# Optimization experiments

Measured on AMD Instinct MI355X. Metric: run time of the kernel, lower is better.

Reference implementation:

```python
import jax, jax.numpy as jnp
import numpy as np

N_NODES = 50000
N_EDGES = 1600000
IN_CH = 256
LAT = 32
HID = 64
OUT_CH = 256
GAT_H = 32  # GAT hidden dims [32, 32], heads=1


def setup_inputs() -> dict:
    key = jax.random.key(0)
    ks = jax.random.split(key, 30)
    nrm = lambda k, shape, s=0.05: jax.random.normal(k, shape, dtype=jnp.float32) * s
    inp = {}
    inp["x"] = jax.random.normal(ks[0], (N_NODES, IN_CH), dtype=jnp.float32)
    inp["edge_index"] = jax.random.randint(ks[1], (2, N_EDGES), 0, N_NODES)
    # GAT layer 1: IN_CH -> 32 (heads=1), layer 2: 32 -> 32, final linear 32 -> LAT
    inp["W_g1"] = nrm(ks[2], (IN_CH, GAT_H)); inp["as_g1"] = nrm(ks[3], (GAT_H,)); inp["ad_g1"] = nrm(ks[4], (GAT_H,)); inp["b_g1"] = jnp.zeros((GAT_H,), jnp.float32)
    inp["W_g2"] = nrm(ks[5], (GAT_H, GAT_H)); inp["as_g2"] = nrm(ks[6], (GAT_H,)); inp["ad_g2"] = nrm(ks[7], (GAT_H,)); inp["b_g2"] = jnp.zeros((GAT_H,), jnp.float32)
    inp["W_gf"] = nrm(ks[8], (GAT_H, LAT)); inp["b_gf"] = jnp.zeros((LAT,), jnp.float32)
    inp["W_m1"] = nrm(ks[9], (IN_CH, HID)); inp["b_m1"] = jnp.zeros((HID,), jnp.float32); inp["g_m1"] = jnp.ones((HID,), jnp.float32); inp["be_m1"] = jnp.zeros((HID,), jnp.float32)
    inp["W_m2"] = nrm(ks[10], (HID, HID)); inp["b_m2"] = jnp.zeros((HID,), jnp.float32); inp["g_m2"] = jnp.ones((HID,), jnp.float32); inp["be_m2"] = jnp.zeros((HID,), jnp.float32)
    inp["W_m3"] = nrm(ks[11], (HID, LAT)); inp["b_m3"] = jnp.zeros((LAT,), jnp.float32); inp["g_m3"] = jnp.ones((LAT,), jnp.float32); inp["be_m3"] = jnp.zeros((LAT,), jnp.float32)
    # final linear LAT -> OUT_CH + ReLU
    inp["W_f"] = nrm(ks[12], (LAT, OUT_CH)); inp["b_f"] = jnp.zeros((OUT_CH,), jnp.float32)
    return inp


def _bn_relu(h, g, b):
    # BatchNorm1d in training mode: batch stats, biased variance, eps=1e-5
    m = jnp.mean(h, axis=0)
    v = jnp.var(h, axis=0)
    return jax.nn.relu((h - m) * jax.lax.rsqrt(v + 1e-5) * g + b)


def _gat(h_in, src, dst, W, a_s, a_d, b):
    # PyG GATConv (heads=1): edge (src j -> dst i), e = LeakyReLU(a_src.Wx_j + a_dst.Wx_i)
    N = h_in.shape[0]
    h = h_in @ W                                   # [N, F]
    e = jax.nn.leaky_relu((h @ a_s)[src] + (h @ a_d)[dst], 0.2)  # [E]
    m = jax.ops.segment_max(e, dst, num_segments=N)              # scatter-softmax over incoming edges
    ex = jnp.exp(e - m[dst])
    den = jax.ops.segment_sum(ex, dst, num_segments=N)
    alpha = ex / den[dst]
    out = jax.ops.segment_sum(alpha[:, None] * h[src], dst, num_segments=N)
    return out + b


def reference(x, edge_index, W_g1, as_g1, ad_g1, b_g1, W_g2, as_g2, ad_g2, b_g2, W_gf, b_gf, W_m1, b_m1, g_m1, be_m1, W_m2, b_m2, g_m2, be_m2, W_m3, b_m3, g_m3, be_m3, W_f, b_f):
    N = x.shape[0]
    loops = jnp.arange(N)
    src = jnp.concatenate([edge_index[0], loops])  # PyG add_self_loops=True
    dst = jnp.concatenate([edge_index[1], loops])
    r = _bn_relu(x @ W_m1 + b_m1, g_m1, be_m1)
    r = _bn_relu(r @ W_m2 + b_m2, g_m2, be_m2)
    r = _bn_relu(r @ W_m3 + b_m3, g_m3, be_m3)
    # GAT interpolation branch (dropout inactive in eval)
    h = jax.nn.relu(_gat(x, src, dst, W_g1, as_g1, ad_g1, b_g1))
    h = jax.nn.relu(_gat(h, src, dst, W_g2, as_g2, ad_g2, b_g2))
    h = h @ W_gf + b_gf
    # blend with alphas = 0.5 constant vector
    out = 0.5 * r + 0.5 * h
    return jax.nn.relu(out @ W_f + b_f)
```

## Files before the change

### kernel.cpp

```cpp
#include <hip/hip_runtime.h>

#define NNODES 50000
#define NEDGES 1600000
#define NBUCK 196
#define BIN_CH 4096
#define CNT_CH 4096

typedef __attribute__((ext_vector_type(4))) float f32x4;
typedef __attribute__((ext_vector_type(8))) short short8;

__device__ __forceinline__ float leaky02(float x) { return x > 0.f ? x : 0.2f * x; }

__device__ __forceinline__ int block_incl_scan(int v, int* sh) {
  int t = threadIdx.x;
  sh[t] = v;
  __syncthreads();
  for (int d = 1; d < 256; d <<= 1) {
    int u = (t >= d) ? sh[t - d] : 0;
    __syncthreads();
    sh[t] += u;
    __syncthreads();
  }
  return sh[t];
}

__global__ __launch_bounds__(256) void k_b0(const int* __restrict__ dst,
                                            int* __restrict__ gcnt, int E) {
  __shared__ int hist[256];
  int t = threadIdx.x;
  hist[t] = 0;
  __syncthreads();
  int base0 = blockIdx.x * CNT_CH;
#pragma unroll
  for (int r = 0; r < CNT_CH / 256; ++r) {
    int idx = base0 + r * 256 + t;
    if (idx < E) atomicAdd(&hist[dst[idx] >> 8], 1);
  }
  __syncthreads();
  if (t < NBUCK && hist[t]) atomicAdd(&gcnt[t], hist[t]);
}

__global__ __launch_bounds__(256) void k_b1(const int* __restrict__ gcnt,
                                            int* __restrict__ base,
                                            int* __restrict__ cursor) {
  __shared__ int sh[256];
  int t = threadIdx.x;
  int v = (t < NBUCK) ? gcnt[t] : 0;
  int incl = block_incl_scan(v, sh);
  if (t < NBUCK) {
    base[t] = incl - v;
    cursor[t] = incl - v;
  }
  if (t == 255) base[NBUCK] = NEDGES;
}

__global__ __launch_bounds__(256) void k_bin(const int* __restrict__ src,
                                             const int* __restrict__ dst,
                                             int* __restrict__ cursor,
                                             unsigned* __restrict__ binned, int E) {
  __shared__ int hist[256];
  __shared__ int cur[256];
  int t = threadIdx.x;
  int base0 = blockIdx.x * BIN_CH;
  unsigned pk[BIN_CH / 256];
  hist[t] = 0;
  __syncthreads();
#pragma unroll
  for (int r = 0; r < BIN_CH / 256; ++r) {
    int idx = base0 + r * 256 + t;
    if (idx < E) {
      unsigned p = ((unsigned)dst[idx] << 16) | (unsigned)src[idx];
      pk[r] = p;
      atomicAdd(&hist[p >> 24], 1);
    }
  }
  __syncthreads();
  if (t < NBUCK && hist[t]) cur[t] = atomicAdd(&cursor[t], hist[t]);
  __syncthreads();
#pragma unroll
  for (int r = 0; r < BIN_CH / 256; ++r) {
    int idx = base0 + r * 256 + t;
    if (idx < E) {
      unsigned p = pk[r];
      int pos = atomicAdd(&cur[p >> 24], 1);
      binned[pos] = p;
    }
  }
}

__global__ __launch_bounds__(256) void k_sort(const unsigned* __restrict__ binned,
                                              const int* __restrict__ base,
                                              int* __restrict__ deg,
                                              int* __restrict__ offs,
                                              int* __restrict__ csr) {
  __shared__ int hist[256];
  __shared__ int scanbuf[256];
  __shared__ int cur[256];
  int t = threadIdx.x;
  int b = blockIdx.x;
  int lo = base[b], hi = base[b + 1];
  int node0 = b << 8;
  hist[t] = 0;
  __syncthreads();
  for (int i = lo + t; i < hi; i += 256)
    atomicAdd(&hist[(binned[i] >> 16) & 255], 1);
  __syncthreads();
  int h = hist[t];
  int incl = block_incl_scan(h, scanbuf);
  int excl = incl - h;
  int node = node0 + t;
  if (node < NNODES) {
    deg[node] = h;
    offs[node] = lo + excl;
  }
  cur[t] = lo + excl;
  __syncthreads();
  for (int i = lo + t; i < hi; i += 256) {
    unsigned p = binned[i];
    int pos = atomicAdd(&cur[(p >> 16) & 255], 1);
    csr[pos] = (int)(p & 0xFFFFu);
  }
}

template <int K, int NC, int TN, int SPLIT, bool BN, bool STATS, int ROWS>
__global__ __launch_bounds__(256) void k_gemm(
    const float* __restrict__ A, const float* __restrict__ bn_sum,
    const float* __restrict__ bn_sq, const float* __restrict__ bn_gamma,
    const float* __restrict__ bn_beta, float invM,
    const float* __restrict__ B0, const float* __restrict__ B1,
    const float* __restrict__ bias0,
    float* __restrict__ out0, float* __restrict__ out1,
    float* __restrict__ gsum, float* __restrict__ gsq, int M) {
  constexpr int KC = 64;
  constexpr int RPT = ROWS / 16;
  __shared__ float As[ROWS * KC];
  __shared__ float Bs[KC * NC];
  __shared__ float scS[BN ? K : 4];
  __shared__ float shS[BN ? K : 4];
  const int tid = threadIdx.x;
  const int row0 = blockIdx.x * ROWS;
  const int cg = tid & 15;
  const int rowg = (tid >> 4) & 15;
  const int swz = (rowg & 3) << 2;

  if constexpr (BN) {
    if (tid < K) {
      float mean = bn_sum[tid] * invM;
      float var = bn_sq[tid] * invM - mean * mean;
      float rs = rsqrtf(var + 1e-5f);
      float sc = rs * bn_gamma[tid];
      scS[tid] = sc;
      shS[tid] = bn_beta[tid] - mean * sc;
    }
    __syncthreads();
  }

  float acc[RPT][TN];
#pragma unroll
  for (int r = 0; r < RPT; ++r)
#pragma unroll
    for (int j = 0; j < TN; ++j) acc[r][j] = 0.f;

  constexpr int KB = KC / 4;
  for (int k0 = 0; k0 < K; k0 += KC) {
#pragma unroll
    for (int it = 0; it < (ROWS * KB) / 256; ++it) {
      int idx = tid + it * 256;
      int row = idx / KB;
      int kb = idx % KB;
      float4 v = make_float4(0.f, 0.f, 0.f, 0.f);
      int grow = row0 + row;
      if (grow < M) {
        v = *reinterpret_cast<const float4*>(&A[(size_t)grow * K + k0 + kb * 4]);
        if constexpr (BN) {
          int kb4 = k0 + kb * 4;
          float4 sc = *reinterpret_cast<const float4*>(&scS[kb4]);
          float4 sf = *reinterpret_cast<const float4*>(&shS[kb4]);
          v.x = fmaxf(v.x * sc.x + sf.x, 0.f);
          v.y = fmaxf(v.y * sc.y + sf.y, 0.f);
          v.z = fmaxf(v.z * sc.z + sf.z, 0.f);
          v.w = fmaxf(v.w * sc.w + sf.w, 0.f);
        }
      }
      *reinterpret_cast<float4*>(&As[row * KC + ((kb ^ (row & 3)) * 4)]) = v;
    }
    {
      constexpr int KB0 = SPLIT / 4;
#pragma unroll
      for (int it = 0; it < (KC * KB0) / 256; ++it) {
        int idx = tid + it * 256;
        int kk = idx / KB0;
        int cb = idx % KB0;
        float4 v = *reinterpret_cast<const float4*>(&B0[(size_t)(k0 + kk) * SPLIT + cb * 4]);
        *reinterpret_cast<float4*>(&Bs[kk * NC + cb * 4]) = v;
      }
    }
    if constexpr (NC > SPLIT) {
      constexpr int W1 = NC - SPLIT;
      constexpr int KB1 = W1 / 4;
#pragma unroll
      for (int it = 0; it < (KC * KB1) / 256; ++it) {
        int idx = tid + it * 256;
        int kk = idx / KB1;
        int cb = idx % KB1;
        float4 v = *reinterpret_cast<const float4*>(&B1[(size_t)(k0 + kk) * W1 + cb * 4]);
        *reinterpret_cast<float4*>(&Bs[kk * NC + SPLIT + cb * 4]) = v;
      }
    }
    __syncthreads();
    for (int kk = 0; kk < KC; kk += 4) {
      float4 a[RPT];
#pragma unroll
      for (int r = 0; r < RPT; ++r)
        a[r] = *reinterpret_cast<const float4*>(&As[(rowg + 16 * r) * KC + (kk ^ swz)]);
      float b[4][TN];
#pragma unroll
      for (int i = 0; i < 4; ++i)
#pragma unroll
        for (int j = 0; j < TN; ++j) b[i][j] = Bs[(kk + i) * NC + cg * TN + j];
#pragma unroll
      for (int r = 0; r < RPT; ++r)
#pragma unroll
        for (int j = 0; j < TN; ++j) {
          acc[r][j] += a[r].x * b[0][j];
          acc[r][j] += a[r].y * b[1][j];
          acc[r][j] += a[r].z * b[2][j];
          acc[r][j] += a[r].w * b[3][j];
        }
    }
    __syncthreads();
  }
  float bias_r[TN];
#pragma unroll
  for (int j = 0; j < TN; ++j) {
    int c = cg * TN + j;
    bias_r[j] = (c < SPLIT) ? bias0[c] : 0.f;
  }
  float cs[TN], cq[TN];
#pragma unroll
  for (int j = 0; j < TN; ++j) { cs[j] = 0.f; cq[j] = 0.f; }
#pragma unroll
  for (int r = 0; r < RPT; ++r) {
    int grow = row0 + rowg + 16 * r;
    if (grow < M) {
#pragma unroll
      for (int j = 0; j < TN; ++j) {
        int c = cg * TN + j;
        if (c < SPLIT) {
          float v = acc[r][j] + bias_r[j];
          out0[(size_t)grow * SPLIT + c] = v;
          if (STATS) { cs[j] += v; cq[j] += v * v; }
        } else {
          out1[(size_t)grow * (NC - SPLIT) + (c - SPLIT)] = acc[r][j];
        }
      }
    }
  }
  if constexpr (STATS) {
#pragma unroll
    for (int j = 0; j < TN; ++j) {
      cs[j] += __shfl_xor(cs[j], 16);
      cs[j] += __shfl_xor(cs[j], 32);
      cq[j] += __shfl_xor(cq[j], 16);
      cq[j] += __shfl_xor(cq[j], 32);
    }
    float* red = Bs;
    int wave = tid >> 6;
    int lane = tid & 63;
    if (lane < 16) {
#pragma unroll
      for (int j = 0; j < TN; ++j) {
        int c = cg * TN + j;
        if (c < SPLIT) {
          red[wave * 2 * SPLIT + c] = cs[j];
          red[wave * 2 * SPLIT + SPLIT + c] = cq[j];
        }
      }
    }
    __syncthreads();
    if (tid < SPLIT) {
      float s = red[tid] + red[2 * SPLIT + tid] + red[4 * SPLIT + tid] + red[6 * SPLIT + tid];
      atomicAdd(&gsum[tid], s);
    } else if (tid < 2 * SPLIT) {
      int c = tid - SPLIT;
      float q = red[SPLIT + c] + red[3 * SPLIT + c] + red[5 * SPLIT + c] + red[7 * SPLIT + c];
      atomicAdd(&gsq[c], q);
    }
  }
}

__global__ __launch_bounds__(256) void k_bsplit(const float* __restrict__ Wm,
                                                const float* __restrict__ Wg,
                                                unsigned short* __restrict__ Bth,
                                                unsigned short* __restrict__ Btl) {
  int col = blockIdx.x;
  int k = threadIdx.x;
  float v = (col < 64) ? Wm[k * 64 + col] : Wg[k * 32 + (col - 64)];
  unsigned b = __float_as_uint(v);
  unsigned h = b & 0xffff0000u;
  float lo = v - __uint_as_float(h);
  Bth[col * 256 + k] = (unsigned short)(h >> 16);
  Btl[col * 256 + k] = (unsigned short)(__float_as_uint(lo) >> 16);
}

union U16 { uint4 u; short8 s; };
__device__ __forceinline__ short8 as_s8(uint4 u) { U16 t; t.u = u; return t.s; }

__device__ __forceinline__ void split2(float x0, float x1, unsigned& h, unsigned& l) {
  unsigned b0 = __float_as_uint(x0), b1 = __float_as_uint(x1);
  unsigned h0 = b0 & 0xffff0000u, h1 = b1 & 0xffff0000u;
  h = (h0 >> 16) | h1;
  float l0 = x0 - __uint_as_float(h0);
  float l1 = x1 - __uint_as_float(h1);
  l = (__float_as_uint(l0) >> 16) | (__float_as_uint(l1) & 0xffff0000u);
}

__device__ __forceinline__ void split8(const float4& a, const float4& b,
                                       short8& hi, short8& lo) {
  uint4 h, l;
  split2(a.x, a.y, h.x, l.x);
  split2(a.z, a.w, h.y, l.y);
  split2(b.x, b.y, h.z, l.z);
  split2(b.z, b.w, h.w, l.w);
  hi = as_s8(h);
  lo = as_s8(l);
}

__global__ __launch_bounds__(256, 2) void k_gemm1_mfma(
    const float* __restrict__ A, const unsigned short* __restrict__ Bth,
    const unsigned short* __restrict__ Btl, const float* __restrict__ bias0,
    float* __restrict__ out0, float* __restrict__ out1,
    float* __restrict__ gsum, float* __restrict__ gsq, int M) {
  __shared__ float red[512];
  const int tid = threadIdx.x;
  const int wv = tid >> 6;
  const int lane = tid & 63;
  const int lg = lane >> 4;
  const int lc = lane & 15;
  const int rowb = blockIdx.x * 128 + wv * 32;

  const int r0 = rowb + lc;
  const int r1 = rowb + 16 + lc;
  const bool v0ok = r0 < M, v1ok = r1 < M;
  const float* a0p = A + (size_t)r0 * 256 + lg * 8;
  const float* a1p = A + (size_t)r1 * 256 + lg * 8;
  const unsigned short* bhp = Bth + (size_t)lc * 256 + lg * 8;
  const unsigned short* blp = Btl + (size_t)lc * 256 + lg * 8;
  const float4 fz = make_float4(0.f, 0.f, 0.f, 0.f);

  float4 araw[2][2][2];
  uint4 bhr[2][6], blr[2][6];
  f32x4 acc[2][6];
#pragma unroll
  for (int rf = 0; rf < 2; ++rf)
#pragma unroll
    for (int cf = 0; cf < 6; ++cf) acc[rf][cf] = (f32x4){0.f, 0.f, 0.f, 0.f};

#pragma unroll
  for (int c = 0; c < 9; ++c) {
    if (c < 8) {
      const int buf = c & 1;
      const int off = c * 32;
      araw[buf][0][0] = v0ok ? *reinterpret_cast<const float4*>(a0p + off) : fz;
      araw[buf][0][1] = v0ok ? *reinterpret_cast<const float4*>(a0p + off + 4) : fz;
      araw[buf][1][0] = v1ok ? *reinterpret_cast<const float4*>(a1p + off) : fz;
      araw[buf][1][1] = v1ok ? *reinterpret_cast<const float4*>(a1p + off + 4) : fz;
#pragma unroll
      for (int cf = 0; cf < 6; ++cf) {
        bhr[buf][cf] = *reinterpret_cast<const uint4*>(bhp + cf * 4096 + off);
        blr[buf][cf] = *reinterpret_cast<const uint4*>(blp + cf * 4096 + off);
      }
    }
    if (c > 0) {
      const int buf = (c - 1) & 1;
      short8 ah[2], al[2], bh[6], bl[6];
#pragma unroll
      for (int rf = 0; rf < 2; ++rf)
        split8(araw[buf][rf][0], araw[buf][rf][1], ah[rf], al[rf]);
#pragma unroll
      for (int cf = 0; cf < 6; ++cf) {
        bh[cf] = as_s8(bhr[buf][cf]);
        bl[cf] = as_s8(blr[buf][cf]);
      }
#pragma unroll
      for (int rf = 0; rf < 2; ++rf)
#pragma unroll
        for (int cf = 0; cf < 6; ++cf) {
          acc[rf][cf] = __builtin_amdgcn_mfma_f32_16x16x32_bf16(ah[rf], bh[cf], acc[rf][cf], 0, 0, 0);
          acc[rf][cf] = __builtin_amdgcn_mfma_f32_16x16x32_bf16(al[rf], bh[cf], acc[rf][cf], 0, 0, 0);
          acc[rf][cf] = __builtin_amdgcn_mfma_f32_16x16x32_bf16(ah[rf], bl[cf], acc[rf][cf], 0, 0, 0);
        }
    }
  }

  float bias_r[4];
#pragma unroll
  for (int cf = 0; cf < 4; ++cf) bias_r[cf] = bias0[cf * 16 + lc];
  float cs[4] = {0.f, 0.f, 0.f, 0.f}, cq[4] = {0.f, 0.f, 0.f, 0.f};
#pragma unroll
  for (int rf = 0; rf < 2; ++rf) {
    int rbase = rowb + rf * 16 + lg * 4;
#pragma unroll
    for (int i = 0; i < 4; ++i) {
      int row = rbase + i;
      if (row < M) {
#pragma unroll
        for (int cf = 0; cf < 4; ++cf) {
          float v = acc[rf][cf][i] + bias_r[cf];
          out0[(size_t)row * 64 + cf * 16 + lc] = v;
          cs[cf] += v;
          cq[cf] += v * v;
        }
#pragma unroll
        for (int cf = 4; cf < 6; ++cf)
          out1[(size_t)row * 32 + (cf - 4) * 16 + lc] = acc[rf][cf][i];
      }
    }
  }
#pragma unroll
  for (int cf = 0; cf < 4; ++cf) {
    cs[cf] += __shfl_xor(cs[cf], 16);
    cs[cf] += __shfl_xor(cs[cf], 32);
    cq[cf] += __shfl_xor(cq[cf], 16);
    cq[cf] += __shfl_xor(cq[cf], 32);
  }
  if (lg == 0) {
#pragma unroll
    for (int cf = 0; cf < 4; ++cf) {
      red[wv * 128 + cf * 16 + lc] = cs[cf];
      red[wv * 128 + 64 + cf * 16 + lc] = cq[cf];
    }
  }
  __syncthreads();
  if (tid < 64) {
    float s = red[tid] + red[128 + tid] + red[256 + tid] + red[384 + tid];
    atomicAdd(&gsum[tid], s);
  } else if (tid < 128) {
    int cc = tid - 64;
    float q = red[64 + cc] + red[192 + cc] + red[320 + cc] + red[448 + cc];
    atomicAdd(&gsq[cc], q);
  }
}

__global__ __launch_bounds__(256) void k_sdot(const float* __restrict__ g,
                                              const float* __restrict__ as_,
                                              const float* __restrict__ ad_,
                                              float* __restrict__ sv,
                                              float* __restrict__ dv, int N) {
  int lane = threadIdx.x & 31;
  int row = blockIdx.x * 8 + (threadIdx.x >> 5);
  if (row >= N) return;
  float v = g[(size_t)row * 32 + lane];
  float a = v * as_[lane];
  float b = v * ad_[lane];
#pragma unroll
  for (int w = 16; w >= 1; w >>= 1) {
    a += __shfl_xor(a, w);
    b += __shfl_xor(b, w);
  }
  if (lane == 0) {
    sv[row] = a;
    dv[row] = b;
  }
}

__global__ __launch_bounds__(256) void k_gat_agg(
    const float* __restrict__ h, const float* __restrict__ sv,
    const float* __restrict__ dv, const int* __restrict__ offs,
    const int* __restrict__ deg, const int* __restrict__ csr,
    const float* __restrict__ bias, float* __restrict__ out, int N) {
  int lane = threadIdx.x & 31;
  int node = blockIdx.x * 8 + (threadIdx.x >> 5);
  if (node >= N) return;
  int start = offs[node];
  int cnt = deg[node];
  float di = dv[node];
  float ex0 = __expf(leaky02(sv[node] + di));
  float den = ex0;
  float acc = ex0 * h[(size_t)node * 32 + lane];
  int k = 0;
  for (; k + 8 <= cnt; k += 8) {
    int j0 = csr[start + k + 0], j1 = csr[start + k + 1];
    int j2 = csr[start + k + 2], j3 = csr[start + k + 3];
    int j4 = csr[start + k + 4], j5 = csr[start + k + 5];
    int j6 = csr[start + k + 6], j7 = csr[start + k + 7];
    float s0 = sv[j0], s1 = sv[j1], s2 = sv[j2], s3 = sv[j3];
    float s4 = sv[j4], s5 = sv[j5], s6 = sv[j6], s7 = sv[j7];
    float h0 = h[(size_t)j0 * 32 + lane], h1 = h[(size_t)j1 * 32 + lane];
    float h2 = h[(size_t)j2 * 32 + lane], h3 = h[(size_t)j3 * 32 + lane];
    float h4 = h[(size_t)j4 * 32 + lane], h5 = h[(size_t)j5 * 32 + lane];
    float h6 = h[(size_t)j6 * 32 + lane], h7 = h[(size_t)j7 * 32 + lane];
    float e0 = __expf(leaky02(s0 + di)), e1 = __expf(leaky02(s1 + di));
    float e2 = __expf(leaky02(s2 + di)), e3 = __expf(leaky02(s3 + di));
    float e4 = __expf(leaky02(s4 + di)), e5 = __expf(leaky02(s5 + di));
    float e6 = __expf(leaky02(s6 + di)), e7 = __expf(leaky02(s7 + di));
    den += ((e0 + e1) + (e2 + e3)) + ((e4 + e5) + (e6 + e7));
    acc += e0 * h0 + e1 * h1 + e2 * h2 + e3 * h3;
    acc += e4 * h4 + e5 * h5 + e6 * h6 + e7 * h7;
  }
  for (; k < cnt; ++k) {
    int j = csr[start + k];
    float ex = __expf(leaky02(sv[j] + di));
    den += ex;
    acc += ex * h[(size_t)j * 32 + lane];
  }
  out[(size_t)node * 32 + lane] = fmaxf(acc / den + bias[lane], 0.f);
}

__global__ __launch_bounds__(256) void k_small_gemm_sd(
    const float* __restrict__ hin, const float* __restrict__ W,
    const float* __restrict__ as_, const float* __restrict__ ad_,
    float* __restrict__ gout, float* __restrict__ sv, float* __restrict__ dv,
    int N) {
  __shared__ float Ws[32][32];
  {
    int t = threadIdx.x;
#pragma unroll
    for (int r = 0; r < 4; ++r) {
      int idx = t + r * 256;
      Ws[idx >> 5][idx & 31] = W[idx];
    }
  }
  __syncthreads();
  int lane = threadIdx.x & 31;
  int row = blockIdx.x * 8 + (threadIdx.x >> 5);
  if (row >= N) return;
  float hv = hin[(size_t)row * 32 + lane];
  float acc = 0.f;
#pragma unroll
  for (int k = 0; k < 32; ++k) acc += __shfl(hv, k, 32) * Ws[k][lane];
  gout[(size_t)row * 32 + lane] = acc;
  float a = acc * as_[lane];
  float b = acc * ad_[lane];
#pragma unroll
  for (int w = 16; w >= 1; w >>= 1) {
    a += __shfl_xor(a, w);
    b += __shfl_xor(b, w);
  }
  if (lane == 0) {
    sv[row] = a;
    dv[row] = b;
  }
}

__global__ __launch_bounds__(256) void k_final2(
    const float* __restrict__ mlp3, const float* __restrict__ sum3,
    const float* __restrict__ sq3, const float* __restrict__ g3,
    const float* __restrict__ be3, float invM, const float* __restrict__ h2,
    const float* __restrict__ Wgf, const float* __restrict__ bgf,
    const float* __restrict__ Wf, const float* __restrict__ bf,
    float* __restrict__ out, int N) {
  __shared__ float WfS[32 * 256];
  __shared__ float Bl[64][36];
  __shared__ float WgfS[32][33];
  __shared__ float colS[3][32];
  const int t = threadIdx.x;
  const int row0 = blockIdx.x * 64;

  {
    const float4* src = reinterpret_cast<const float4*>(Wf);
    float4* dst = reinterpret_cast<float4*>(WfS);
#pragma unroll
    for (int r = 0; r < 8; ++r) dst[t + r * 256] = src[t + r * 256];
  }
#pragma unroll
  for (int r = 0; r < 4; ++r) {
    int idx = t + r * 256;
    WgfS[idx >> 5][idx & 31] = Wgf[idx];
  }
  if (t < 32) {
    float mean = sum3[t] * invM;
    float var = sq3[t] * invM - mean * mean;
    float rs = rsqrtf(var + 1e-5f);
    float sc = rs * g3[t];
    colS[0][t] = sc;
    colS[1][t] = be3[t] - mean * sc;
    colS[2][t] = bgf[t];
  }
#pragma unroll
  for (int r = 0; r < 2; ++r) {
    int idx = t + r * 256;
    int row = idx >> 3;
    int k4 = idx & 7;
    int grow = row0 + row;
    float4 v = make_float4(0.f, 0.f, 0.f, 0.f);
    if (grow < N) v = *reinterpret_cast<const float4*>(&h2[(size_t)grow * 32 + k4 * 4]);
    *reinterpret_cast<float4*>(&Bl[row][k4 * 4]) = v;
  }
  __syncthreads();

  const int col = t & 31;
  const int rb = t >> 5;
  float w[32];
#pragma unroll
  for (int k = 0; k < 32; ++k) w[k] = WgfS[k][col];
  float bl[8];
#pragma unroll
  for (int r = 0; r < 8; ++r) {
    int row = rb + 8 * r;
    float a = colS[2][col];
#pragma unroll
    for (int k4 = 0; k4 < 8; ++k4) {
      float4 hv = *reinterpret_cast<const float4*>(&Bl[row][k4 * 4]);
      a += hv.x * w[k4 * 4 + 0] + hv.y * w[k4 * 4 + 1] +
           hv.z * w[k4 * 4 + 2] + hv.w * w[k4 * 4 + 3];
    }
    int grow = row0 + row;
    float pre = (grow < N) ? mlp3[(size_t)grow * 32 + col] : 0.f;
    float rv = fmaxf(pre * colS[0][col] + colS[1][col], 0.f);
    bl[r] = 0.5f * rv + 0.5f * a;
  }
  __syncthreads();
#pragma unroll
  for (int r = 0; r < 8; ++r) Bl[rb + 8 * r][col] = bl[r];
  __syncthreads();

  const int cg = t & 31;
  const int rowg = t >> 5;
  const float4* Wf4 = reinterpret_cast<const float4*>(WfS);
  float4 acc0[8], acc1[8];
#pragma unroll
  for (int r = 0; r < 8; ++r) {
    acc0[r] = make_float4(0.f, 0.f, 0.f, 0.f);
    acc1[r] = make_float4(0.f, 0.f, 0.f, 0.f);
  }
  for (int k = 0; k < 32; k += 4) {
    float4 a[8];
#pragma unroll
    for (int r = 0; r < 8; ++r)
      a[r] = *reinterpret_cast<const float4*>(&Bl[rowg + 8 * r][k]);
    float4 b0[4], b1[4];
#pragma unroll
    for (int i = 0; i < 4; ++i) {
      b0[i] = Wf4[(k + i) * 64 + cg];
      b1[i] = Wf4[(k + i) * 64 + cg + 32];
    }
#pragma unroll
    for (int r = 0; r < 8; ++r) {
      float av[4] = {a[r].x, a[r].y, a[r].z, a[r].w};
#pragma unroll
      for (int i = 0; i < 4; ++i) {
        acc0[r].x += av[i] * b0[i].x;
        acc0[r].y += av[i] * b0[i].y;
        acc0[r].z += av[i] * b0[i].z;
        acc0[r].w += av[i] * b0[i].w;
        acc1[r].x += av[i] * b1[i].x;
        acc1[r].y += av[i] * b1[i].y;
        acc1[r].z += av[i] * b1[i].z;
        acc1[r].w += av[i] * b1[i].w;
      }
    }
  }
  float4 bfA = reinterpret_cast<const float4*>(bf)[cg];
  float4 bfB = reinterpret_cast<const float4*>(bf)[cg + 32];
  float4* out4 = reinterpret_cast<float4*>(out);
#pragma unroll
  for (int r = 0; r < 8; ++r) {
    int grow = row0 + rowg + 8 * r;
    if (grow < N) {
      float4 o0 = acc0[r], o1 = acc1[r];
      o0.x = fmaxf(o0.x + bfA.x, 0.f); o0.y = fmaxf(o0.y + bfA.y, 0.f);
      o0.z = fmaxf(o0.z + bfA.z, 0.f); o0.w = fmaxf(o0.w + bfA.w, 0.f);
      o1.x = fmaxf(o1.x + bfB.x, 0.f); o1.y = fmaxf(o1.y + bfB.y, 0.f);
      o1.z = fmaxf(o1.z + bfB.z, 0.f); o1.w = fmaxf(o1.w + bfB.w, 0.f);
      out4[(size_t)grow * 64 + cg] = o0;
      out4[(size_t)grow * 64 + cg + 32] = o1;
    }
  }
}

extern "C" void kernel_launch(void* const* d_in, const int* in_sizes, int n_in,
                              void* d_out, int out_size, void* d_ws, size_t ws_size,
                              hipStream_t stream) {
  const float* x = (const float*)d_in[0];
  const int* edge = (const int*)d_in[1];
  const float* W_g1 = (const float*)d_in[2];
  const float* as_g1 = (const float*)d_in[3];
  const float* ad_g1 = (const float*)d_in[4];
  const float* b_g1 = (const float*)d_in[5];
  const float* W_g2 = (const float*)d_in[6];
  const float* as_g2 = (const float*)d_in[7];
  const float* ad_g2 = (const float*)d_in[8];
  const float* b_g2 = (const float*)d_in[9];
  const float* W_gf = (const float*)d_in[10];
  const float* b_gf = (const float*)d_in[11];
  const float* W_m1 = (const float*)d_in[12];
  const float* b_m1 = (const float*)d_in[13];
  const float* g_m1 = (const float*)d_in[14];
  const float* be_m1 = (const float*)d_in[15];
  const float* W_m2 = (const float*)d_in[16];
  const float* b_m2 = (const float*)d_in[17];
  const float* g_m2 = (const float*)d_in[18];
  const float* be_m2 = (const float*)d_in[19];
  const float* W_m3 = (const float*)d_in[20];
  const float* b_m3 = (const float*)d_in[21];
  const float* g_m3 = (const float*)d_in[22];
  const float* be_m3 = (const float*)d_in[23];
  const float* W_f = (const float*)d_in[24];
  const float* b_f = (const float*)d_in[25];
  float* out = (float*)d_out;

  const int N = NNODES, E = NEDGES;
  const float invM = 1.f / N;
  const int* esrc = edge;
  const int* edst = edge + E;

  float* ws = (float*)d_ws;
  float* g1 = ws;
  float* mlp1 = g1 + (size_t)N * 32;
  float* mlp2 = mlp1 + (size_t)N * 64;
  float* mlp3 = mlp2 + (size_t)N * 64;
  float* h1 = mlp3 + (size_t)N * 32;
  float* g2 = h1 + (size_t)N * 32;
  float* h2 = g2 + (size_t)N * 32;
  float* s1 = h2 + (size_t)N * 32;
  float* d1 = s1 + N;
  float* s2 = d1 + N;
  float* d2 = s2 + N;
  float* stats = d2 + N;
  float* sum1 = stats, *sq1 = stats + 64;
  float* sum2 = stats + 128, *sq2 = stats + 192;
  float* sum3 = stats + 256, *sq3 = stats + 288;
  int* ip = (int*)(stats + 384);
  int* gcnt = ip;
  int* base = gcnt + 256;
  int* cursor = base + 256;
  int* deg = cursor + 256;
  int* offs = deg + N;
  int* csr = offs + N;
  unsigned* binned = (unsigned*)mlp2;
  unsigned short* Bth = (unsigned short*)((char*)mlp2 + (size_t)E * 4);
  unsigned short* Btl = Bth + 96 * 256;

  hipMemsetAsync(gcnt, 0, 256 * sizeof(int), stream);
  hipMemsetAsync(stats, 0, 384 * sizeof(float), stream);

  k_bsplit<<<96, 256, 0, stream>>>(W_m1, W_g1, Bth, Btl);

  k_b0<<<(E + CNT_CH - 1) / CNT_CH, 256, 0, stream>>>(edst, gcnt, E);
  k_b1<<<1, 256, 0, stream>>>(gcnt, base, cursor);
  k_bin<<<(E + BIN_CH - 1) / BIN_CH, 256, 0, stream>>>(esrc, edst, cursor, binned, E);
  k_sort<<<NBUCK, 256, 0, stream>>>(binned, base, deg, offs, csr);

  const int GB128 = (N + 127) / 128;

  k_gemm1_mfma<<<GB128, 256, 0, stream>>>(x, Bth, Btl, b_m1, mlp1, g1, sum1, sq1, N);
  k_sdot<<<(N + 7) / 8, 256, 0, stream>>>(g1, as_g1, ad_g1, s1, d1, N);
  k_gat_agg<<<(N + 7) / 8, 256, 0, stream>>>(g1, s1, d1, offs, deg, csr, b_g1, h1, N);

  k_gemm<64, 64, 4, 64, true, true, 128><<<GB128, 256, 0, stream>>>(
      mlp1, sum1, sq1, g_m1, be_m1, invM, W_m2, nullptr, b_m2,
      mlp2, nullptr, sum2, sq2, N);

  k_small_gemm_sd<<<(N + 7) / 8, 256, 0, stream>>>(h1, W_g2, as_g2, ad_g2, g2, s2, d2, N);
  k_gat_agg<<<(N + 7) / 8, 256, 0, stream>>>(g2, s2, d2, offs, deg, csr, b_g2, h2, N);

  k_gemm<64, 32, 2, 32, true, true, 128><<<GB128, 256, 0, stream>>>(
      mlp2, sum2, sq2, g_m2, be_m2, invM, W_m3, nullptr, b_m3,
      mlp3, nullptr, sum3, sq3, N);

  k_final2<<<(N + 63) / 64, 256, 0, stream>>>(mlp3, sum3, sq3, g_m3, be_m3, invM,
                                              h2, W_gf, b_gf, W_f, b_f, out, N);
}
```

Before: 420.2 us.

## Stage GEMM1 A tiles through LDS via global_load_lds with swizzle

The first fused GEMM now stages x tiles into double-buffered LDS using direct global-to-LDS loads with an XOR swizzle, instead of each lane loading its own rows into registers. The split weights are pre-packed in a fragment-ordered layout so each lane reads them with contiguous 16-byte loads. Blocks shrink to 128 threads over 64 rows. The aim is coalesced A loads and lower register pressure, at the cost of a barrier per K-step and more blocks issuing atomics.

```diff
diff --git a/kernel.cpp b/kernel.cpp
--- a/kernel.cpp
+++ b/kernel.cpp
@@ -289,18 +289,22 @@
   }
 }
 
-__global__ __launch_bounds__(256) void k_bsplit(const float* __restrict__ Wm,
+__global__ __launch_bounds__(512) void k_bsplit(const float* __restrict__ Wm,
                                                 const float* __restrict__ Wg,
-                                                unsigned short* __restrict__ Bth,
-                                                unsigned short* __restrict__ Btl) {
-  int col = blockIdx.x;
-  int k = threadIdx.x;
+                                                unsigned short* __restrict__ Bt) {
+  int b = blockIdx.x;
+  int c = b / 6, cf = b % 6;
+  int t = threadIdx.x;
+  int lane = t >> 3, j = t & 7;
+  int lg = lane >> 4, lc = lane & 15;
+  int k = c * 32 + lg * 8 + j;
+  int col = cf * 16 + lc;
   float v = (col < 64) ? Wm[k * 64 + col] : Wg[k * 32 + (col - 64)];
-  unsigned b = __float_as_uint(v);
-  unsigned h = b & 0xffff0000u;
+  unsigned bb = __float_as_uint(v);
+  unsigned h = bb & 0xffff0000u;
   float lo = v - __uint_as_float(h);
-  Bth[col * 256 + k] = (unsigned short)(h >> 16);
-  Btl[col * 256 + k] = (unsigned short)(__float_as_uint(lo) >> 16);
+  Bt[(size_t)(b * 2 + 0) * 512 + t] = (unsigned short)(h >> 16);
+  Bt[(size_t)(b * 2 + 1) * 512 + t] = (unsigned short)(__float_as_uint(lo) >> 16);
 }
 
 union U16 { uint4 u; short8 s; };
@@ -326,30 +330,34 @@
   lo = as_s8(l);
 }
 
-__global__ __launch_bounds__(256, 2) void k_gemm1_mfma(
-    const float* __restrict__ A, const unsigned short* __restrict__ Bth,
-    const unsigned short* __restrict__ Btl, const float* __restrict__ bias0,
+__device__ __forceinline__ void gload16(const float* g, float* l) {
+  __builtin_amdgcn_global_load_lds(
+      (const __attribute__((address_space(1))) void*)g,
+      (__attribute__((address_space(3))) void*)l, 16, 0, 0);
+}
+
+__global__ __launch_bounds__(128) void k_gemm1_mfma(
+    const float* __restrict__ A, const unsigned short* __restrict__ Bt,
+    const float* __restrict__ bias0,
     float* __restrict__ out0, float* __restrict__ out1,
     float* __restrict__ gsum, float* __restrict__ gsq, int M) {
-  __shared__ float red[512];
+  __shared__ float As[2][64 * 32];
+  __shared__ float red[256];
   const int tid = threadIdx.x;
   const int wv = tid >> 6;
   const int lane = tid & 63;
   const int lg = lane >> 4;
   const int lc = lane & 15;
-  const int rowb = blockIdx.x * 128 + wv * 32;
-
-  const int r0 = rowb + lc;
-  const int r1 = rowb + 16 + lc;
-  const bool v0ok = r0 < M, v1ok = r1 < M;
-  const float* a0p = A + (size_t)r0 * 256 + lg * 8;
-  const float* a1p = A + (size_t)r1 * 256 + lg * 8;
-  const unsigned short* bhp = Bth + (size_t)lc * 256 + lg * 8;
-  const unsigned short* blp = Btl + (size_t)lc * 256 + lg * 8;
-  const float4 fz = make_float4(0.f, 0.f, 0.f, 0.f);
-
-  float4 araw[2][2][2];
-  uint4 bhr[2][6], blr[2][6];
+  const int rowb = blockIdx.x * 64;
+
+  const int srow = lane >> 3;
+  const int sslot = (lane & 7) ^ srow;
+
+  const int rl0 = wv * 32 + lc;
+  const int rl1 = rl0 + 16;
+  const int p00 = (lg * 2) ^ (rl0 & 7), p01 = (lg * 2 + 1) ^ (rl0 & 7);
+  const int p10 = (lg * 2) ^ (rl1 & 7), p11 = (lg * 2 + 1) ^ (rl1 & 7);
+
   f32x4 acc[2][6];
 #pragma unroll
   for (int rf = 0; rf < 2; ++rf)
@@ -357,40 +365,51 @@
     for (int cf = 0; cf < 6; ++cf) acc[rf][cf] = (f32x4){0.f, 0.f, 0.f, 0.f};
 
 #pragma unroll
-  for (int c = 0; c < 9; ++c) {
-    if (c < 8) {
-      const int buf = c & 1;
-      const int off = c * 32;
-      araw[buf][0][0] = v0ok ? *reinterpret_cast<const float4*>(a0p + off) : fz;
-      araw[buf][0][1] = v0ok ? *reinterpret_cast<const float4*>(a0p + off + 4) : fz;
-      araw[buf][1][0] = v1ok ? *reinterpret_cast<const float4*>(a1p + off) : fz;
-      araw[buf][1][1] = v1ok ? *reinterpret_cast<const float4*>(a1p + off + 4) : fz;
+  for (int it = 0; it < 4; ++it) {
+    const int si = wv * 4 + it;
+    int grow = rowb + si * 8 + srow;
+    grow = grow < M ? grow : M - 1;
+    gload16(A + (size_t)grow * 256 + sslot * 4, &As[0][si * 256]);
+  }
+  __syncthreads();
+
+#pragma unroll
+  for (int c = 0; c < 8; ++c) {
+    const int buf = c & 1;
+    if (c < 7) {
+#pragma unroll
+      for (int it = 0; it < 4; ++it) {
+        const int si = wv * 4 + it;
+        int grow = rowb + si * 8 + srow;
+        grow = grow < M ? grow : M - 1;
+        gload16(A + (size_t)grow * 256 + (c + 1) * 32 + sslot * 4,
+                &As[buf ^ 1][si * 256]);
+      }
+    }
+    uint4 bhr[6], blr[6];
+    const unsigned short* bp = Bt + (size_t)c * 6144 + lane * 8;
+#pragma unroll
+    for (int cf = 0; cf < 6; ++cf) {
+      bhr[cf] = *reinterpret_cast<const uint4*>(bp + cf * 1024);
+      blr[cf] = *reinterpret_cast<const uint4*>(bp + cf * 1024 + 512);
+    }
+    float4 a00 = *reinterpret_cast<const float4*>(&As[buf][rl0 * 32 + p00 * 4]);
+    float4 a01 = *reinterpret_cast<const float4*>(&As[buf][rl0 * 32 + p01 * 4]);
+    float4 a10 = *reinterpret_cast<const float4*>(&As[buf][rl1 * 32 + p10 * 4]);
+    float4 a11 = *reinterpret_cast<const float4*>(&As[buf][rl1 * 32 + p11 * 4]);
+    short8 ah[2], al[2];
+    split8(a00, a01, ah[0], al[0]);
+    split8(a10, a11, ah[1], al[1]);
+#pragma unroll
+    for (int rf = 0; rf < 2; ++rf)
 #pragma unroll
       for (int cf = 0; cf < 6; ++cf) {
-        bhr[buf][cf] = *reinterpret_cast<const uint4*>(bhp + cf * 4096 + off);
-        blr[buf][cf] = *reinterpret_cast<const uint4*>(blp + cf * 4096 + off);
-      }
-    }
-    if (c > 0) {
-      const int buf = (c - 1) & 1;
-      short8 ah[2], al[2], bh[6], bl[6];
-#pragma unroll
-      for (int rf = 0; rf < 2; ++rf)
-        split8(araw[buf][rf][0], araw[buf][rf][1], ah[rf], al[rf]);
-#pragma unroll
-      for (int cf = 0; cf < 6; ++cf) {
-        bh[cf] = as_s8(bhr[buf][cf]);
-        bl[cf] = as_s8(blr[buf][cf]);
-      }
-#pragma unroll
-      for (int rf = 0; rf < 2; ++rf)
-#pragma unroll
-        for (int cf = 0; cf < 6; ++cf) {
-          acc[rf][cf] = __builtin_amdgcn_mfma_f32_16x16x32_bf16(ah[rf], bh[cf], acc[rf][cf], 0, 0, 0);
-          acc[rf][cf] = __builtin_amdgcn_mfma_f32_16x16x32_bf16(al[rf], bh[cf], acc[rf][cf], 0, 0, 0);
-          acc[rf][cf] = __builtin_amdgcn_mfma_f32_16x16x32_bf16(ah[rf], bl[cf], acc[rf][cf], 0, 0, 0);
-        }
-    }
+        short8 bh = as_s8(bhr[cf]), bl = as_s8(blr[cf]);
+        acc[rf][cf] = __builtin_amdgcn_mfma_f32_16x16x32_bf16(ah[rf], bh, acc[rf][cf], 0, 0, 0);
+        acc[rf][cf] = __builtin_amdgcn_mfma_f32_16x16x32_bf16(al[rf], bh, acc[rf][cf], 0, 0, 0);
+        acc[rf][cf] = __builtin_amdgcn_mfma_f32_16x16x32_bf16(ah[rf], bl, acc[rf][cf], 0, 0, 0);
+      }
+    __syncthreads();
   }
 
   float bias_r[4];
@@ -399,7 +418,7 @@
   float cs[4] = {0.f, 0.f, 0.f, 0.f}, cq[4] = {0.f, 0.f, 0.f, 0.f};
 #pragma unroll
   for (int rf = 0; rf < 2; ++rf) {
-    int rbase = rowb + rf * 16 + lg * 4;
+    int rbase = rowb + wv * 32 + rf * 16 + lg * 4;
 #pragma unroll
     for (int i = 0; i < 4; ++i) {
       int row = rbase + i;
@@ -433,12 +452,10 @@
   }
   __syncthreads();
   if (tid < 64) {
-    float s = red[tid] + red[128 + tid] + red[256 + tid] + red[384 + tid];
-    atomicAdd(&gsum[tid], s);
-  } else if (tid < 128) {
+    atomicAdd(&gsum[tid], red[tid] + red[128 + tid]);
+  } else {
     int cc = tid - 64;
-    float q = red[64 + cc] + red[192 + cc] + red[320 + cc] + red[448 + cc];
-    atomicAdd(&gsq[cc], q);
+    atomicAdd(&gsq[cc], red[64 + cc] + red[192 + cc]);
   }
 }
 
@@ -729,22 +746,22 @@
   int* offs = deg + N;
   int* csr = offs + N;
   unsigned* binned = (unsigned*)mlp2;
-  unsigned short* Bth = (unsigned short*)((char*)mlp2 + (size_t)E * 4);
-  unsigned short* Btl = Bth + 96 * 256;
+  unsigned short* Bt = (unsigned short*)((char*)mlp2 + (size_t)E * 4);
 
   hipMemsetAsync(gcnt, 0, 256 * sizeof(int), stream);
   hipMemsetAsync(stats, 0, 384 * sizeof(float), stream);
 
-  k_bsplit<<<96, 256, 0, stream>>>(W_m1, W_g1, Bth, Btl);
+  k_bsplit<<<48, 512, 0, stream>>>(W_m1, W_g1, Bt);
 
   k_b0<<<(E + CNT_CH - 1) / CNT_CH, 256, 0, stream>>>(edst, gcnt, E);
   k_b1<<<1, 256, 0, stream>>>(gcnt, base, cursor);
   k_bin<<<(E + BIN_CH - 1) / BIN_CH, 256, 0, stream>>>(esrc, edst, cursor, binned, E);
   k_sort<<<NBUCK, 256, 0, stream>>>(binned, base, deg, offs, csr);
 
+  const int GB64 = (N + 63) / 64;
   const int GB128 = (N + 127) / 128;
 
-  k_gemm1_mfma<<<GB128, 256, 0, stream>>>(x, Bth, Btl, b_m1, mlp1, g1, sum1, sq1, N);
+  k_gemm1_mfma<<<GB64, 128, 0, stream>>>(x, Bt, b_m1, mlp1, g1, sum1, sq1, N);
   k_sdot<<<(N + 7) / 8, 256, 0, stream>>>(g1, as_g1, ad_g1, s1, d1, N);
   k_gat_agg<<<(N + 7) / 8, 256, 0, stream>>>(g1, s1, d1, offs, deg, csr, b_g1, h1, N);
 
```

Measured after the change: 398.2 us. 5.2% less time.
